# Kernel optimization log

Hardware: AMD Instinct MI355X
Metric: run time of the kernel (lower is better)

The kernel has to match this reference:

```python
import jax, jax.numpy as jnp
import numpy as np

NUM_HEADS = 16
NEG_INF = -1e9  # matches torch source's -1000000000.0 additive mask
ROPE_BASE = 10000.0


def _rope(t):
    """Rotary position embedding, half-rotation form. t: [B, H, S, D]."""
    D = t.shape[-1]
    S = t.shape[2]
    inv_freq = 1.0 / (ROPE_BASE ** (jnp.arange(0, D, 2, dtype=jnp.float32) / D))  # [D/2]
    pos = jnp.arange(S, dtype=jnp.float32)
    freqs = pos[:, None] * inv_freq[None, :]          # [S, D/2]
    cos = jnp.cos(freqs)[None, None]                  # [1,1,S,D/2]
    sin = jnp.sin(freqs)[None, None]
    t1, t2 = t[..., : D // 2], t[..., D // 2 :]
    return jnp.concatenate([t1 * cos - t2 * sin, t1 * sin + t2 * cos], axis=-1)


def setup_inputs() -> dict:
    key = jax.random.key(0)
    kx, kq, kk, kv, ko = jax.random.split(key, 5)
    B, S, Dm = 2, 2048, 1024
    w_scale = 0.02
    return {
        "x": jax.random.normal(kx, (B, S, Dm), dtype=jnp.float32),
        "attention_mask": jnp.ones((B, S), dtype=jnp.float32),
        "Wq": jax.random.normal(kq, (Dm, Dm), dtype=jnp.float32) * w_scale,
        "Wk": jax.random.normal(kk, (Dm, Dm), dtype=jnp.float32) * w_scale,
        "Wv": jax.random.normal(kv, (Dm, Dm), dtype=jnp.float32) * w_scale,
        "Wo": jax.random.normal(ko, (Dm, Dm), dtype=jnp.float32) * w_scale,
    }


def reference(x, attention_mask, Wq, Wk, Wv, Wo):
    B, S, Dm = x.shape
    H = NUM_HEADS
    Hd = Dm // H

    def to_heads(t):  # [B,S,Dm] -> [B,H,S,Hd]
        return t.reshape(B, S, H, Hd).transpose(0, 2, 1, 3)

    q = _rope(to_heads(x @ Wq))
    k = _rope(to_heads(x @ Wk))
    v = to_heads(x @ Wv)

    scaling = 1.0 / np.sqrt(Hd).astype(np.float32)
    scores = jnp.einsum("bhqd,bhkd->bhqk", q, k) * scaling  # [B,H,S,S]

    # causal additive mask (triu of -1e9 above diagonal), as in apply_masking
    causal = jnp.triu(jnp.full((S, S), NEG_INF, dtype=scores.dtype), k=1)
    # padding mask: (1 - mask) * -1e9 broadcast to [B,1,1,S]
    amask = (1.0 - attention_mask)[:, None, None, :] * NEG_INF
    scores = scores + causal[None, None] + amask

    weights = jax.nn.softmax(scores, axis=-1)
    out = jnp.einsum("bhqk,bhkd->bhqd", weights, v)  # [B,H,S,Hd]
    out = out.transpose(0, 2, 1, 3).reshape(B, S, Dm)
    return out @ Wo
```

## Files before the change

kernel.cpp:

```cpp
#include <hip/hip_runtime.h>

typedef unsigned short u16;
typedef unsigned int u32;
typedef __attribute__((ext_vector_type(8))) short short8;
typedef __attribute__((ext_vector_type(4))) short s4v;
typedef __attribute__((ext_vector_type(4))) float f32x4;

#define S_LEN 2048
#define NH 16
#define HD 64
#define DM 1024

#if __has_builtin(__builtin_amdgcn_mfma_f32_16x16x16_bf16)
#define MFMA_K16(a, b, c) __builtin_amdgcn_mfma_f32_16x16x16_bf16(a, b, c, 0, 0, 0)
#else
#define MFMA_K16(a, b, c) __builtin_amdgcn_mfma_f32_16x16x16bf16_1k(a, b, c, 0, 0, 0)
#endif

__device__ __forceinline__ u16 f2bf(float f) {
    union { float f; u32 u; } v; v.f = f;
    u32 u = v.u;
    u32 r = u + 0x7fffu + ((u >> 16) & 1u);
    return (u16)(r >> 16);
}
__device__ __forceinline__ float bf2f(u16 h) {
    union { u32 u; float f; } v; v.u = ((u32)h) << 16;
    return v.f;
}

__device__ __forceinline__ u32 cvtpk_bf16(float lo, float hi) {
    u32 r;
    asm("v_cvt_pk_bf16_f32 %0, %1, %2" : "=v"(r) : "v"(lo), "v"(hi));
    return r;
}

__device__ __forceinline__ void load_lds16(const u16* g, u16* l) {
    __builtin_amdgcn_global_load_lds((const __attribute__((address_space(1))) void*)g,
                                     (__attribute__((address_space(3))) void*)l, 16, 0, 0);
}

__global__ __launch_bounds__(256) void cvt_bf16(const float* __restrict__ in, u16* __restrict__ out, int n) {
    int i = (blockIdx.x * 256 + threadIdx.x) * 4;
    if (i < n) {
        float4 v = *(const float4*)(in + i);
        ushort4 o;
        o.x = f2bf(v.x); o.y = f2bf(v.y); o.z = f2bf(v.z); o.w = f2bf(v.w);
        *(ushort4*)(out + i) = o;
    }
}

__global__ __launch_bounds__(256) void transpose_w4(const float* __restrict__ W0, const float* __restrict__ W1,
                                                    const float* __restrict__ W2, const float* __restrict__ W3,
                                                    u16* __restrict__ T0, u16* __restrict__ T1,
                                                    u16* __restrict__ T2, u16* __restrict__ T3) {
    __shared__ float tile[32][33];
    int z = blockIdx.z;
    const float* W = (z == 0) ? W0 : (z == 1) ? W1 : (z == 2) ? W2 : W3;
    u16* Wt = (z == 0) ? T0 : (z == 1) ? T1 : (z == 2) ? T2 : T3;
    int tx = threadIdx.x, ty = threadIdx.y;
    int k0 = blockIdx.y * 32, n0 = blockIdx.x * 32;
    #pragma unroll
    for (int j = 0; j < 32; j += 8)
        tile[ty + j][tx] = W[(size_t)(k0 + ty + j) * DM + n0 + tx];
    __syncthreads();
    #pragma unroll
    for (int j = 0; j < 32; j += 8)
        Wt[(size_t)(n0 + ty + j) * DM + k0 + tx] = f2bf(tile[tx][ty + j]);
}

template<int MODE, int NI>
__global__ __launch_bounds__(256) void gemm128(const u16* __restrict__ A, const u16* __restrict__ Bt,
                                               u16* __restrict__ Qh, u16* __restrict__ Kh,
                                               u16* __restrict__ Vh, float* __restrict__ Cf) {
    __shared__ u16 Al[128 * 64];
    __shared__ u16 Bl[NI * 32 * 64];
    const int K = DM;
    int tid = threadIdx.x;
    int wave = tid >> 6, lane = tid & 63, g = lane >> 4, ln = lane & 15;
    int wm = (wave >> 1) * 64, wn = (wave & 1) * (NI * 16);
    size_t mb0 = (size_t)blockIdx.y * 128, nb0 = (size_t)blockIdx.x * (NI * 32);

    f32x4 acc[4][NI];
    #pragma unroll
    for (int i = 0; i < 4; i++)
        #pragma unroll
        for (int j = 0; j < NI; j++)
            acc[i][j] = (f32x4){0.f, 0.f, 0.f, 0.f};

    int srow = lane >> 3;
    int scol = (lane & 7) ^ srow;
    const u16* Ag = A + (mb0 + wave * 32 + srow) * K + scol * 8;
    u16* Alw = Al + wave * 2048;
    const u16* Bg;
    u16* Blw;
    if (NI == 4) {
        Bg = Bt + (nb0 + wave * 32 + srow) * K + scol * 8;
        Blw = Bl + wave * 2048;
    } else {
        Bg = Bt + (nb0 + wave * 16 + srow) * K + scol * 8;
        Blw = Bl + wave * 1024;
    }
    int cswz = ln & 7;

    for (int k0 = 0; k0 < K; k0 += 64) {
        __syncthreads();
        #pragma unroll
        for (int c = 0; c < 4; c++)
            load_lds16(Ag + (size_t)(c * 8) * K + k0, Alw + c * 512);
        #pragma unroll
        for (int c = 0; c < (NI == 4 ? 4 : 2); c++)
            load_lds16(Bg + (size_t)(c * 8) * K + k0, Blw + c * 512);
        __syncthreads();
        short8 af[2][4], bf[2][NI];
        #pragma unroll
        for (int ks = 0; ks < 2; ks++) {
            #pragma unroll
            for (int i = 0; i < 4; i++)
                af[ks][i] = *(const short8*)&Al[(wm + i * 16 + ln) * 64 + (((ks * 4 + g) ^ cswz) * 8)];
            #pragma unroll
            for (int i = 0; i < NI; i++)
                bf[ks][i] = *(const short8*)&Bl[(wn + i * 16 + ln) * 64 + (((ks * 4 + g) ^ cswz) * 8)];
        }
        #pragma unroll
        for (int ks = 0; ks < 2; ks++)
            #pragma unroll
            for (int mi = 0; mi < 4; mi++)
                #pragma unroll
                for (int ni = 0; ni < NI; ni++)
                    acc[mi][ni] = __builtin_amdgcn_mfma_f32_16x16x32_bf16(af[ks][mi], bf[ks][ni], acc[mi][ni], 0, 0, 0);
    }

    if (MODE == 1) {
        #pragma unroll
        for (int mi = 0; mi < 4; mi++)
            #pragma unroll
            for (int ni = 0; ni < NI; ni++)
                #pragma unroll
                for (int r = 0; r < 4; r++) {
                    int m = (int)mb0 + wm + mi * 16 + g * 4 + r;
                    int n = (int)nb0 + wn + ni * 16 + ln;
                    Cf[(size_t)m * DM + n] = acc[mi][ni][r];
                }
    } else {
        int nbase = (int)nb0 + wn;
        int which = nbase >> 10;
        int h = (nbase & (DM - 1)) >> 6;
        if (which < 2) {
            u16* dst = (which == 0) ? Qh : Kh;
            float inv0 = exp2f(-0.4152408746976557f * (float)ln);
            float inv1 = exp2f(-0.4152408746976557f * (float)(16 + ln));
            #pragma unroll
            for (int mi = 0; mi < 4; mi++) {
                #pragma unroll
                for (int r = 0; r < 4; r++) {
                    int m = (int)mb0 + wm + mi * 16 + g * 4 + r;
                    int b = m >> 11, s = m & (S_LEN - 1);
                    float fs = (float)s;
                    float sn0, cs0, sn1, cs1;
                    __sincosf(fs * inv0, &sn0, &cs0);
                    __sincosf(fs * inv1, &sn1, &cs1);
                    float a0 = acc[mi][0][r], a1 = acc[mi][1][r];
                    float a2 = acc[mi][2][r], a3 = acc[mi][3][r];
                    size_t base = ((size_t)(b * NH + h) * S_LEN + s) * HD;
                    dst[base + ln]      = f2bf(a0 * cs0 - a2 * sn0);
                    dst[base + 16 + ln] = f2bf(a1 * cs1 - a3 * sn1);
                    dst[base + 32 + ln] = f2bf(a0 * sn0 + a2 * cs0);
                    dst[base + 48 + ln] = f2bf(a1 * sn1 + a3 * cs1);
                }
            }
        } else {
            #pragma unroll
            for (int mi = 0; mi < 4; mi++) {
                #pragma unroll
                for (int r = 0; r < 4; r++) {
                    int m = (int)mb0 + wm + mi * 16 + g * 4 + r;
                    int b = m >> 11, s = m & (S_LEN - 1);
                    size_t base = ((size_t)(b * NH + h) * S_LEN + s) * HD;
                    #pragma unroll
                    for (int ni = 0; ni < 4; ni++)
                        Vh[base + ni * 16 + ln] = f2bf(acc[mi][ni][r]);
                }
            }
        }
    }
}

__global__ __launch_bounds__(256) void vtrans(const u16* __restrict__ Vh, u16* __restrict__ Vt) {
    __shared__ u16 t[64][70];
    int tid = threadIdx.x;
    int s0 = blockIdx.x * 64, bh = blockIdx.y;
    int r = tid >> 2, c = (tid & 3) * 8;
    const u16* src = Vh + ((size_t)bh * S_LEN + s0) * HD;
    *(short8*)&t[r][c]      = *(const short8*)(src + (size_t)r * HD + c);
    *(short8*)&t[r][c + 32] = *(const short8*)(src + (size_t)r * HD + c + 32);
    __syncthreads();
    u16* dst = Vt + ((size_t)bh * HD + r) * S_LEN + s0;
    short8 o0, o1;
    #pragma unroll
    for (int j = 0; j < 8; j++) {
        o0[j] = (short)t[c + j][r];
        o1[j] = (short)t[c + 32 + j][r];
    }
    *(short8*)(dst + c)      = o0;
    *(short8*)(dst + c + 32) = o1;
}

__global__ __launch_bounds__(512, 4) void flash_kernel(const u16* __restrict__ Qh, const u16* __restrict__ Kh,
                                                       const u16* __restrict__ Vt, const float* __restrict__ amask,
                                                       u16* __restrict__ Op0, u16* __restrict__ Op1,
                                                       u16* __restrict__ Op2, u16* __restrict__ Op3,
                                                       float* __restrict__ L0, float* __restrict__ L1,
                                                       float* __restrict__ L2, float* __restrict__ L3) {
    __shared__ u16 Kl[2][64 * 64];
    __shared__ u16 Vl[2][64 * 64];
    __shared__ float Ml[2][64];
    int tid = threadIdx.x;
    int wave = tid >> 6, lane = tid & 63, g = lane >> 4, ln = lane & 15;
    int i = (int)blockIdx.x;
    int xcd = i & 7;
    int j = i >> 3;
    int bh = xcd * 4 + (j >> 6);
    int inner = j & 63;
    int qblk = 15 - (inner >> 2);
    int sp = inner & 3;
    int b = bh >> 4;
    int q0 = qblk * 128 + wave * 16;
    int qv = q0 + ln;
    const u16* Qb = Qh + (size_t)bh * (S_LEN * HD);
    const u16* Kb = Kh + (size_t)bh * (S_LEN * HD);
    const u16* Vb = Vt + (size_t)bh * (S_LEN * HD);
    const float* am = amask + b * S_LEN;

    short8 qa0 = *(const short8*)(Qb + (size_t)(q0 + ln) * HD + g * 8);
    short8 qa1 = *(const short8*)(Qb + (size_t)(q0 + ln) * HD + 32 + g * 8);

    f32x4 O[4];
    #pragma unroll
    for (int i2 = 0; i2 < 4; i2++) O[i2] = (f32x4){0.f, 0.f, 0.f, 0.f};
    float lsum = 0.f;
    const float SCL = 0.125f * 1.4426950408889634f;
    const float MSCL = -1.4426950408889634e9f;

    int T = 2 * qblk + 2;
    int srow = tid >> 3, scid = tid & 7, s7 = srow & 7;
    int stoff = srow * 64 + ((scid ^ s7) * 8);
    const u16* KgL = Kb + (size_t)srow * HD + ((scid ^ s7) * 8);
    const u16* VgP = Vb + (size_t)srow * S_LEN + scid * 8;
    bool vswap = (wave & 1);

    int l7 = ln & 7;
    int kc0 = (g ^ l7) * 8;
    int kc1 = ((4 + g) ^ l7) * 8;
    int rbq = ln * 64;
    int vcoff[4];
    #pragma unroll
    for (int n0 = 0; n0 < 4; n0++)
        vcoff[n0] = (((n0 * 2 + (g >> 1)) ^ l7) * 8) + ((((g & 1) ^ (ln >> 3)) & 1) * 4);

    load_lds16(KgL + (size_t)(sp * 64) * HD, &Kl[0][wave * 512]);
    short8 vR = *(const short8*)(VgP + sp * 64);
    float mR = 0.f;
    if (tid < 64) mR = (1.0f - am[sp * 64 + tid]) * MSCL;
    int cur = 0;

    for (int kt = sp; kt < T; kt += 4) {
        int kbase = kt * 64;
        short8 vS = vR;
        if (vswap) vS = __builtin_shufflevector(vR, vR, 4, 5, 6, 7, 0, 1, 2, 3);
        *(short8*)(Vl[cur] + stoff) = vS;
        if (tid < 64) Ml[cur][tid] = mR;
        __syncthreads();

        if (kt + 4 < T) {
            load_lds16(KgL + (size_t)(kbase + 256) * HD, &Kl[cur ^ 1][wave * 512]);
            vR = *(const short8*)(VgP + (kbase + 256));
            if (tid < 64) mR = (1.0f - am[kbase + 256 + tid]) * MSCL;
        }

        if (kbase <= q0 + 15) {
            const u16* Klc = Kl[cur];
            const u16* Vlc = Vl[cur];
            u32 pk[4][2];
            bool needmask = (kbase + 63 > q0);

            if (!needmask) {
                #pragma unroll
                for (int n0 = 0; n0 < 4; n0++) {
                    const u16* kr = Klc + (n0 * 16) * 64 + rbq;
                    short8 kb0 = *(const short8*)(kr + kc0);
                    short8 kb1 = *(const short8*)(kr + kc1);
                    f32x4 sv = (f32x4){0.f, 0.f, 0.f, 0.f};
                    sv = __builtin_amdgcn_mfma_f32_16x16x32_bf16(kb0, qa0, sv, 0, 0, 0);
                    sv = __builtin_amdgcn_mfma_f32_16x16x32_bf16(kb1, qa1, sv, 0, 0, 0);
                    f32x4 mkv = *(f32x4*)&Ml[cur][n0 * 16 + g * 4];
                    float p[4];
                    #pragma unroll
                    for (int r = 0; r < 4; r++) {
                        p[r] = exp2f(sv[r] * SCL + mkv[r]);
                        lsum += p[r];
                    }
                    pk[n0][0] = cvtpk_bf16(p[0], p[1]);
                    pk[n0][1] = cvtpk_bf16(p[2], p[3]);
                }
            } else {
                #pragma unroll
                for (int n0 = 0; n0 < 4; n0++) {
                    const u16* kr = Klc + (n0 * 16) * 64 + rbq;
                    short8 kb0 = *(const short8*)(kr + kc0);
                    short8 kb1 = *(const short8*)(kr + kc1);
                    f32x4 sv = (f32x4){0.f, 0.f, 0.f, 0.f};
                    sv = __builtin_amdgcn_mfma_f32_16x16x32_bf16(kb0, qa0, sv, 0, 0, 0);
                    sv = __builtin_amdgcn_mfma_f32_16x16x32_bf16(kb1, qa1, sv, 0, 0, 0);
                    f32x4 mkv = *(f32x4*)&Ml[cur][n0 * 16 + g * 4];
                    int keyb = kbase + n0 * 16 + g * 4;
                    float p[4];
                    #pragma unroll
                    for (int r = 0; r < 4; r++) {
                        float s2 = sv[r] * SCL + mkv[r];
                        if (keyb + r > qv) s2 = -1.0e9f;
                        p[r] = exp2f(s2);
                        lsum += p[r];
                    }
                    pk[n0][0] = cvtpk_bf16(p[0], p[1]);
                    pk[n0][1] = cvtpk_bf16(p[2], p[3]);
                }
            }

            __builtin_amdgcn_s_setprio(1);
            #pragma unroll
            for (int t = 0; t < 4; t++) {
                const u16* vr = Vlc + (t * 16) * 64 + rbq;
                #pragma unroll
                for (int n0 = 0; n0 < 4; n0++) {
                    s4v va = *(const s4v*)(vr + vcoff[n0]);
                    union { u32 u[2]; s4v v; } pb;
                    pb.u[0] = pk[n0][0];
                    pb.u[1] = pk[n0][1];
                    O[t] = MFMA_K16(va, pb.v, O[t]);
                }
            }
            __builtin_amdgcn_s_setprio(0);
        }
        cur ^= 1;
    }

    lsum += __shfl_xor(lsum, 16, 64);
    lsum += __shfl_xor(lsum, 32, 64);
    u16* Od = (sp == 0) ? Op0 : (sp == 1) ? Op1 : (sp == 2) ? Op2 : Op3;
    float* Ld = (sp == 0) ? L0 : (sp == 1) ? L1 : (sp == 2) ? L2 : L3;
    if (lane < 16) Ld[(size_t)bh * S_LEN + q0 + ln] = lsum;
    size_t obase = (size_t)bh * (HD * S_LEN) + q0 + ln;
    #pragma unroll
    for (int t = 0; t < 4; t++)
        #pragma unroll
        for (int r = 0; r < 4; r++)
            Od[obase + (size_t)(t * 16 + g * 4 + r) * S_LEN] = f2bf(O[t][r]);
}

__global__ __launch_bounds__(256) void flash_reduce(const u16* __restrict__ Op0, const u16* __restrict__ Op1,
                                                    const u16* __restrict__ Op2, const u16* __restrict__ Op3,
                                                    const float* __restrict__ L0, const float* __restrict__ L1,
                                                    const float* __restrict__ L2, const float* __restrict__ L3,
                                                    u16* __restrict__ attn) {
    __shared__ float t[64][65];
    int tid = threadIdx.x;
    int qt = blockIdx.x, bh = blockIdx.y;
    int b = bh >> 4, h = bh & (NH - 1);
    #pragma unroll
    for (int it = 0; it < 2; it++) {
        int idx = tid + it * 256;
        int d = idx >> 3, c = (idx & 7) * 8;
        size_t off = (size_t)bh * (HD * S_LEN) + (size_t)d * S_LEN + qt * 64 + c;
        short8 a0 = *(const short8*)(Op0 + off);
        short8 a1 = *(const short8*)(Op1 + off);
        short8 a2 = *(const short8*)(Op2 + off);
        short8 a3 = *(const short8*)(Op3 + off);
        #pragma unroll
        for (int j = 0; j < 8; j++)
            t[d][c + j] = bf2f((u16)a0[j]) + bf2f((u16)a1[j]) + bf2f((u16)a2[j]) + bf2f((u16)a3[j]);
    }
    __syncthreads();
    int qr = tid >> 2, dc = (tid & 3) * 16;
    int qg = qt * 64 + qr;
    size_t li = (size_t)bh * S_LEN + qg;
    float inv = 1.0f / (L0[li] + L1[li] + L2[li] + L3[li]);
    short8 o0, o1;
    #pragma unroll
    for (int j = 0; j < 8; j++) {
        o0[j] = (short)f2bf(t[dc + j][qr] * inv);
        o1[j] = (short)f2bf(t[dc + 8 + j][qr] * inv);
    }
    u16* dst = attn + ((size_t)b * S_LEN + qg) * DM + h * HD + dc;
    *(short8*)dst = o0;
    *(short8*)(dst + 8) = o1;
}

extern "C" void kernel_launch(void* const* d_in, const int* in_sizes, int n_in,
                              void* d_out, int out_size, void* d_ws, size_t ws_size,
                              hipStream_t stream) {
    const float* x     = (const float*)d_in[0];
    const float* amask = (const float*)d_in[1];
    const float* Wq    = (const float*)d_in[2];
    const float* Wk    = (const float*)d_in[3];
    const float* Wv    = (const float*)d_in[4];
    const float* Wo    = (const float*)d_in[5];
    float* out = (float*)d_out;
    char* ws = (char*)d_ws;

    u16* x_bf   = (u16*)(ws);
    u16* Op1    = (u16*)(ws);
    u16* Wqkv_t = (u16*)(ws + 8388608);
    float* L0   = (float*)(ws + 8388608);
    float* L1   = (float*)(ws + 8650752);
    float* L2   = (float*)(ws + 8912896);
    float* L3   = (float*)(ws + 9175040);
    u16* Wo_t   = (u16*)(ws + 14680064);
    u16* Qh     = (u16*)(ws + 16777216);
    u16* Kh     = (u16*)(ws + 25165824);
    u16* Vt     = (u16*)(ws + 33554432);
    u16* attnF  = (u16*)(ws + 33554432);
    u16* Vh     = (u16*)(ws + 41943040);
    u16* Op0    = (u16*)(ws + 41943040);
    u16* Op2    = (u16*)d_out;
    u16* Op3    = (u16*)d_out + 4194304;

    cvt_bf16<<<4096, 256, 0, stream>>>(x, x_bf, 2 * S_LEN * DM);

    transpose_w4<<<dim3(32, 32, 4), dim3(32, 8), 0, stream>>>(
        Wq, Wk, Wv, Wo, Wqkv_t, Wqkv_t + 1048576, Wqkv_t + 2097152, Wo_t);

    gemm128<0, 4><<<dim3(24, 32), 256, 0, stream>>>(x_bf, Wqkv_t, Qh, Kh, Vh, nullptr);

    vtrans<<<dim3(32, 2 * NH), 256, 0, stream>>>(Vh, Vt);

    flash_kernel<<<dim3(2048), 512, 0, stream>>>(Qh, Kh, Vt, amask,
                                                 Op0, Op1, Op2, Op3, L0, L1, L2, L3);

    flash_reduce<<<dim3(32, 2 * NH), 256, 0, stream>>>(Op0, Op1, Op2, Op3,
                                                       L0, L1, L2, L3, attnF);

    gemm128<1, 2><<<dim3(16, 32), 256, 0, stream>>>(attnF, Wo_t, nullptr, nullptr, nullptr, out);
}
```

Before: 196.4 us.

## Double-buffer LDS tiles in gemm128 to prefetch next K-slice during MFMA

```diff
diff --git a/kernel.cpp b/kernel.cpp
--- a/kernel.cpp
+++ b/kernel.cpp
@@ -72,8 +72,8 @@
 __global__ __launch_bounds__(256) void gemm128(const u16* __restrict__ A, const u16* __restrict__ Bt,
                                                u16* __restrict__ Qh, u16* __restrict__ Kh,
                                                u16* __restrict__ Vh, float* __restrict__ Cf) {
-    __shared__ u16 Al[128 * 64];
-    __shared__ u16 Bl[NI * 32 * 64];
+    __shared__ u16 Al[2][128 * 64];
+    __shared__ u16 Bl[2][NI * 32 * 64];
     const int K = DM;
     int tid = threadIdx.x;
     int wave = tid >> 6, lane = tid & 63, g = lane >> 4, ln = lane & 15;
@@ -90,36 +90,47 @@
     int srow = lane >> 3;
     int scol = (lane & 7) ^ srow;
     const u16* Ag = A + (mb0 + wave * 32 + srow) * K + scol * 8;
-    u16* Alw = Al + wave * 2048;
+    int AlwOff = wave * 2048;
     const u16* Bg;
-    u16* Blw;
+    int BlwOff;
     if (NI == 4) {
         Bg = Bt + (nb0 + wave * 32 + srow) * K + scol * 8;
-        Blw = Bl + wave * 2048;
+        BlwOff = wave * 2048;
     } else {
         Bg = Bt + (nb0 + wave * 16 + srow) * K + scol * 8;
-        Blw = Bl + wave * 1024;
+        BlwOff = wave * 1024;
     }
     int cswz = ln & 7;
+
+    #pragma unroll
+    for (int c = 0; c < 4; c++)
+        load_lds16(Ag + (size_t)(c * 8) * K, &Al[0][AlwOff + c * 512]);
+    #pragma unroll
+    for (int c = 0; c < (NI == 4 ? 4 : 2); c++)
+        load_lds16(Bg + (size_t)(c * 8) * K, &Bl[0][BlwOff + c * 512]);
+    int cur = 0;
 
     for (int k0 = 0; k0 < K; k0 += 64) {
         __syncthreads();
-        #pragma unroll
-        for (int c = 0; c < 4; c++)
-            load_lds16(Ag + (size_t)(c * 8) * K + k0, Alw + c * 512);
-        #pragma unroll
-        for (int c = 0; c < (NI == 4 ? 4 : 2); c++)
-            load_lds16(Bg + (size_t)(c * 8) * K + k0, Blw + c * 512);
-        __syncthreads();
+
+        if (k0 + 64 < K) {
+            #pragma unroll
+            for (int c = 0; c < 4; c++)
+                load_lds16(Ag + (size_t)(c * 8) * K + k0 + 64, &Al[cur ^ 1][AlwOff + c * 512]);
+            #pragma unroll
+            for (int c = 0; c < (NI == 4 ? 4 : 2); c++)
+                load_lds16(Bg + (size_t)(c * 8) * K + k0 + 64, &Bl[cur ^ 1][BlwOff + c * 512]);
+        }
+
         short8 af[2][4], bf[2][NI];
         #pragma unroll
         for (int ks = 0; ks < 2; ks++) {
             #pragma unroll
             for (int i = 0; i < 4; i++)
-                af[ks][i] = *(const short8*)&Al[(wm + i * 16 + ln) * 64 + (((ks * 4 + g) ^ cswz) * 8)];
+                af[ks][i] = *(const short8*)&Al[cur][(wm + i * 16 + ln) * 64 + (((ks * 4 + g) ^ cswz) * 8)];
             #pragma unroll
             for (int i = 0; i < NI; i++)
-                bf[ks][i] = *(const short8*)&Bl[(wn + i * 16 + ln) * 64 + (((ks * 4 + g) ^ cswz) * 8)];
+                bf[ks][i] = *(const short8*)&Bl[cur][(wn + i * 16 + ln) * 64 + (((ks * 4 + g) ^ cswz) * 8)];
         }
         #pragma unroll
         for (int ks = 0; ks < 2; ks++)
@@ -128,6 +139,7 @@
                 #pragma unroll
                 for (int ni = 0; ni < NI; ni++)
                     acc[mi][ni] = __builtin_amdgcn_mfma_f32_16x16x32_bf16(af[ks][mi], bf[ks][ni], acc[mi][ni], 0, 0, 0);
+        cur ^= 1;
     }
 
     if (MODE == 1) {
```

New measurement: 203.9 us. 3.8% more time.
